# Kernel tuning notes

Hardware: AMD Instinct MI355X
Metric: run time of the kernel (lower is better)

## Reference

```python
import jax, jax.numpy as jnp
import numpy as np

BS, SEQ, ENC, DEC, HEADS, INTERM = 32, 2048, 512, 512, 8, 128
IH = INTERM * HEADS


def setup_inputs() -> dict:
    key = jax.random.key(0)
    ks = jax.random.split(key, 16)
    s = 0.02
    return {
        "enc": jax.random.normal(ks[0], (BS, SEQ, ENC), jnp.float32),
        "dec": jax.random.normal(ks[1], (BS, 1, DEC + ENC), jnp.float32),
        "kappa": jax.random.uniform(ks[2], (BS, 1, HEADS), jnp.float32),
        "mask": jnp.ones((BS, SEQ, 1), jnp.float32),
        "Wv": jax.random.normal(ks[3], (ENC, IH), jnp.float32) * s,
        "bv": jnp.zeros((IH,), jnp.float32),
        "Wq": jax.random.normal(ks[4], (DEC + ENC, IH), jnp.float32) * s,
        "bq": jnp.zeros((IH,), jnp.float32),
        "Wf": jax.random.normal(ks[5], (IH, HEADS), jnp.float32) * s,
        "bf": jnp.zeros((HEADS,), jnp.float32),
        "Wb": jax.random.normal(ks[6], (DEC + ENC, HEADS), jnp.float32) * s,
        "bb": jnp.zeros((HEADS,), jnp.float32),
        "Wk": jax.random.normal(ks[7], (DEC + ENC, HEADS), jnp.float32) * s,
        "bk": jnp.zeros((HEADS,), jnp.float32),
        "Wfc": jax.random.normal(ks[8], (ENC * HEADS, ENC), jnp.float32) * s,
        "bfc": jnp.zeros((ENC,), jnp.float32),
    }


def reference(enc, dec, kappa, mask, Wv, bv, Wq, bq, Wf, bf, Wb, bb, Wk, bk, Wfc, bfc):
    bs, seq_len, _ = enc.shape
    sp = jax.nn.softplus
    value = enc @ Wv + bv                      # (bs, seq, IH)
    query = dec @ Wq + bq                      # (bs, 1, IH), broadcasts over seq
    alpha = sp(jnp.tanh(query + value) @ Wf + bf) * mask   # (bs, seq, heads)
    beta = sp(dec @ Wb + bb)                   # (bs, 1, heads)
    kappa = kappa + sp(dec @ Wk + bk)          # (bs, 1, heads)
    u = jnp.arange(seq_len, dtype=enc.dtype)[None, :, None]
    score = alpha * jnp.exp(-beta * (kappa - u) ** 2)       # (bs, seq, heads)
    # weighted reduction over seq: (bs, heads, enc) then flatten in heads-major order
    context = jnp.einsum("bsh,bse->bhe", score, enc).reshape(bs, -1)
    context = context @ Wfc + bfc              # (bs, enc)
    return context[:, None, :], kappa, score
```

## Files before the change

### kernel.cpp

```cpp
#include <hip/hip_runtime.h>
#include <cstdint>
#include <cstddef>

#define BSZ    32
#define SEQL   2048
#define ENCD   512
#define DE     1024
#define NHEADS 8
#define IHD    1024

typedef unsigned short u16;
typedef __bf16 bf16x8 __attribute__((ext_vector_type(8)));
typedef float floatx4 __attribute__((ext_vector_type(4)));
typedef unsigned short u16x8 __attribute__((ext_vector_type(8)));

__device__ __forceinline__ u16 f2bf(float f) {
    unsigned int u = __float_as_uint(f);
    u = (u + 0x7FFFu + ((u >> 16) & 1u)) >> 16;
    return (u16)u;
}
__device__ __forceinline__ float bf2f(u16 v) {
    return __uint_as_float(((unsigned int)v) << 16);
}
__device__ __forceinline__ float softplus_f(float x) {
    return fmaxf(x, 0.0f) + log1pf(__expf(-fabsf(x)));
}
__device__ __forceinline__ float tanh_fast(float x) {
    const float e = __expf(2.0f * x);
    return 1.0f - 2.0f / (e + 1.0f);
}
__device__ __forceinline__ void async_cp16(u16* lds, const u16* g) {
    __builtin_amdgcn_global_load_lds(
        (const __attribute__((address_space(1))) unsigned int*)g,
        (__attribute__((address_space(3))) unsigned int*)lds, 16, 0, 0);
}

__global__ __launch_bounds__(256) void pre_kernel(
    const float* __restrict__ Wv, const float* __restrict__ Wf,
    u16* __restrict__ WvT, u16* __restrict__ wfb,
    const float* __restrict__ dec, const float* __restrict__ kappa_in,
    const float* __restrict__ Wq, const float* __restrict__ bq,
    const float* __restrict__ bv,
    const float* __restrict__ Wb, const float* __restrict__ bb,
    const float* __restrict__ Wk, const float* __restrict__ bk,
    float* __restrict__ query_ws, float* __restrict__ beta_ws,
    float* __restrict__ kappa_out)
{
    __shared__ float sh[64 * 65];
    const int bid = blockIdx.x, tid = threadIdx.x;

    if (bid < 128) {
        const int nt = bid & 15, kt = bid >> 4;
        for (int i = tid; i < 4096; i += 256) {
            const int kk = i >> 6, nn = i & 63;
            sh[kk * 65 + nn] = Wv[(size_t)(kt * 64 + kk) * IHD + nt * 64 + nn];
        }
        __syncthreads();
        for (int i = tid; i < 4096; i += 256) {
            const int nn = i >> 6, kk = i & 63;
            WvT[(size_t)(nt * 64 + nn) * 512 + kt * 64 + kk] = f2bf(sh[kk * 65 + nn]);
        }
        return;
    }
    if (bid == 128) {
        for (int i = tid; i < 8192; i += 256) {
            const int j   = i & 7;
            const int fr8 = (i >> 3) & 7;
            const int qd  = (i >> 6) & 3;
            const int ks  = (i >> 8) & 3;
            const int nn  = i >> 10;
            const int row = nn * 128 + ks * 32 + qd * 8 + j;
            wfb[i] = f2bf(Wf[row * NHEADS + fr8]);
        }
        return;
    }
    const int p = bid - 129;
    const int b = p & 31, y = p >> 5;
    float* s_dec = sh;
    float* s_red = sh + DE;
    for (int i = tid; i < DE; i += 256) s_dec[i] = dec[b * DE + i];
    __syncthreads();

    if (y < 32) {
        const int cl = tid & 31, kg = tid >> 5;
        const int col = y * 32 + cl;
        float a = 0.f;
        const float* w = Wq + col;
        #pragma unroll 8
        for (int k = kg * 128; k < kg * 128 + 128; ++k)
            a = fmaf(s_dec[k], w[(size_t)k * IHD], a);
        s_red[tid] = a;
        __syncthreads();
        if (tid < 32) {
            float s = 0.f;
            #pragma unroll
            for (int i = 0; i < 8; ++i) s += s_red[i * 32 + tid];
            query_ws[(size_t)b * IHD + col] = s + bq[col] + bv[col];
        }
    } else {
        const int h = tid & 7, kg = tid >> 3;
        float ab = 0.f, ak = 0.f;
        for (int k = kg * 32; k < kg * 32 + 32; ++k) {
            const float d = s_dec[k];
            ab = fmaf(d, Wb[k * NHEADS + h], ab);
            ak = fmaf(d, Wk[k * NHEADS + h], ak);
        }
        s_red[tid] = ab;
        __syncthreads();
        for (int off = 128; off >= 8; off >>= 1) {
            if (tid < off) s_red[tid] += s_red[tid + off];
            __syncthreads();
        }
        const float abT = (tid < 8) ? s_red[tid] : 0.f;
        __syncthreads();
        s_red[tid] = ak;
        __syncthreads();
        for (int off = 128; off >= 8; off >>= 1) {
            if (tid < off) s_red[tid] += s_red[tid + off];
            __syncthreads();
        }
        if (tid < 8) {
            beta_ws[b * NHEADS + tid]   = softplus_f(bb[tid] + abT);
            kappa_out[b * NHEADS + tid] = kappa_in[b * NHEADS + tid]
                                        + softplus_f(bk[tid] + s_red[tid]);
        }
    }
}

#define BM 128

__global__ __launch_bounds__(256, 2) void gemm_score_ctx_kernel(
    const float* __restrict__ enc, u16* __restrict__ encb,
    const u16* __restrict__ wvT,
    const u16* __restrict__ wfb2, const float* __restrict__ bf_g,
    const float* __restrict__ mask, const float* __restrict__ query_ws,
    const float* __restrict__ beta_ws, const float* __restrict__ kappa_out,
    float* __restrict__ score_out, float* __restrict__ ctx_part)
{
    __shared__ __align__(16) unsigned char smem[69632];
    u16*   tT      = (u16*)(smem + 32768);
    float* s_score = (float*)(smem + 65536);

    const int tid  = threadIdx.x;
    const int m0   = blockIdx.x * BM;
    const int b    = blockIdx.x >> 4;
    const int sc   = blockIdx.x & 15;
    const int lane = tid & 63;
    const int w    = tid >> 6;
    const int wr   = w >> 1, wc = w & 1;
    const int fr   = lane & 15, quad = lane >> 4;

    {
        const float4* src = (const float4*)enc + (size_t)m0 * 128;
        u16x8* dst = (u16x8*)(encb + (size_t)m0 * 512);
        #pragma unroll 4
        for (int i = tid; i < 8192; i += 256) {
            const float4 a = src[i * 2], b2 = src[i * 2 + 1];
            u16x8 o;
            o[0] = f2bf(a.x);  o[1] = f2bf(a.y);  o[2] = f2bf(a.z);  o[3] = f2bf(a.w);
            o[4] = f2bf(b2.x); o[5] = f2bf(b2.y); o[6] = f2bf(b2.z); o[7] = f2bf(b2.w);
            dst[i] = o;
        }
        asm volatile("s_waitcnt vmcnt(0)" ::: "memory");
        __builtin_amdgcn_sched_barrier(0);
        __builtin_amdgcn_s_barrier();
    }

    int mA[4], csA[4];
    #pragma unroll
    for (int r = 0; r < 4; ++r) {
        const int c = r * 256 + tid;
        mA[r]  = c >> 3;
        csA[r] = (c & 7) ^ (mA[r] & 7);
    }

    auto stage = [&](int bufsel, int it) {
        u16* Ab = (u16*)(smem + bufsel * 32768);
        u16* Bb = Ab + 8192;
        const int nn2 = it >> 3, kt2 = it & 7;
        const size_t aoff = (size_t)kt2 * 64;
        const size_t boff = (size_t)nn2 * (128 * 512) + (size_t)kt2 * 64;
        #pragma unroll
        for (int r = 0; r < 4; ++r) {
            async_cp16(Ab + (r * 256 + (tid & 192)) * 8,
                       encb + (size_t)(m0 + mA[r]) * 512 + aoff + csA[r] * 8);
            async_cp16(Bb + (size_t)(r * 256 + (tid & 192)) * 8,
                       wvT + (size_t)mA[r] * 512 + boff + csA[r] * 8);
        }
    };

    floatx4 acc2[2] = {};

    stage(0, 0);

    for (int nn = 0; nn < 8; ++nn) {
        const int n0 = nn * 128;
        float qv[4];
        bf16x8 wfr[4];
        floatx4 acc[4][4] = {};

        #pragma unroll
        for (int kt = 0; kt < 8; ++kt) {
            const int it = nn * 8 + kt;
            if (kt < 7 || nn < 7)
                stage((it + 1) & 1, it + 1);
            if (kt == 0) {
                #pragma unroll
                for (int nt = 0; nt < 4; ++nt)
                    qv[nt] = query_ws[(size_t)b * IHD + n0 + wc * 64 + nt * 16 + fr];
                #pragma unroll
                for (int ks = 0; ks < 4; ++ks)
                    wfr[ks] = *(const bf16x8*)&wfb2[((nn * 4 + ks) * 4 + quad) * 64
                                                    + (fr & 7) * 8];
            }
            if (kt == 7 && nn == 7) {
                asm volatile("s_waitcnt vmcnt(0)" ::: "memory");
            } else if (kt == 0) {
                asm volatile("s_waitcnt vmcnt(16)" ::: "memory");
            } else {
                asm volatile("s_waitcnt vmcnt(8)" ::: "memory");
            }
            __builtin_amdgcn_sched_barrier(0);
            __builtin_amdgcn_s_barrier();

            u16* Ab = (u16*)(smem + (it & 1) * 32768);
            u16* Bb = Ab + 8192;
            __builtin_amdgcn_s_setprio(1);
            #pragma unroll
            for (int s2 = 0; s2 < 2; ++s2) {
                bf16x8 af[4], bfr[4];
                #pragma unroll
                for (int mt = 0; mt < 4; ++mt) {
                    const int ma = wr * 64 + mt * 16 + fr;
                    const int ca = (s2 * 4 + quad) ^ (ma & 7);
                    af[mt] = *(const bf16x8*)&Ab[ma * 64 + ca * 8];
                }
                #pragma unroll
                for (int nt = 0; nt < 4; ++nt) {
                    const int nb = wc * 64 + nt * 16 + fr;
                    const int cb = (s2 * 4 + quad) ^ (nb & 7);
                    bfr[nt] = *(const bf16x8*)&Bb[nb * 64 + cb * 8];
                }
                #pragma unroll
                for (int mt = 0; mt < 4; ++mt)
                    #pragma unroll
                    for (int nt = 0; nt < 4; ++nt)
                        acc[mt][nt] = __builtin_amdgcn_mfma_f32_16x16x32_bf16(
                            af[mt], bfr[nt], acc[mt][nt], 0, 0, 0);
            }
            __builtin_amdgcn_s_setprio(0);
            __builtin_amdgcn_sched_barrier(0);
            __builtin_amdgcn_s_barrier();
        }

        #pragma unroll
        for (int mt = 0; mt < 4; ++mt) {
            #pragma unroll
            for (int nt = 0; nt < 4; ++nt) {
                const int col = wc * 64 + nt * 16 + fr;
                #pragma unroll
                for (int reg = 0; reg < 4; ++reg) {
                    const int row = wr * 64 + mt * 16 + quad * 4 + reg;
                    ((__bf16*)tT)[row * 128 + (col ^ ((row & 7) << 3))] =
                        (__bf16)tanh_fast(acc[mt][nt][reg] + qv[nt]);
                }
            }
        }
        asm volatile("s_waitcnt lgkmcnt(0)" ::: "memory");
        __builtin_amdgcn_sched_barrier(0);
        __builtin_amdgcn_s_barrier();

        #pragma unroll
        for (int t = 0; t < 2; ++t) {
            const int row = w * 32 + t * 16 + fr;
            #pragma unroll
            for (int ks = 0; ks < 4; ++ks) {
                const bf16x8 ta = *(const bf16x8*)
                    &tT[row * 128 + ((ks * 32 + quad * 8) ^ ((row & 7) << 3))];
                acc2[t] = __builtin_amdgcn_mfma_f32_16x16x32_bf16(ta, wfr[ks], acc2[t], 0, 0, 0);
            }
        }
        __builtin_amdgcn_sched_barrier(0);
        __builtin_amdgcn_s_barrier();
    }

    if (fr < NHEADS) {
        const float bfh = bf_g[fr];
        const float bet = beta_ws[b * NHEADS + fr];
        const float kap = kappa_out[b * NHEADS + fr];
        #pragma unroll
        for (int t = 0; t < 2; ++t) {
            #pragma unroll
            for (int reg = 0; reg < 4; ++reg) {
                const int row  = w * 32 + t * 16 + quad * 4 + reg;
                const int grow = m0 + row;
                const int s = grow & 2047;
                const float alpha = softplus_f(acc2[t][reg] + bfh) * mask[grow];
                const float du = kap - (float)s;
                s_score[row * NHEADS + fr] = alpha * __expf(-bet * du * du);
            }
        }
    }
    asm volatile("s_waitcnt lgkmcnt(0)" ::: "memory");
    __builtin_amdgcn_s_barrier();

    {
        const float4* src4 = (const float4*)s_score;
        float4* dst4 = (float4*)(score_out + (size_t)m0 * NHEADS);
        dst4[tid] = src4[tid];
    }

    {
        float acc0[8] = {}, acc1[8] = {};
        const u16* ep = encb + (size_t)m0 * 512 + lane * 8;
        for (int s0 = 0; s0 < 128; s0 += 16) {
            u16x8 ev[16];
            #pragma unroll
            for (int u = 0; u < 16; ++u)
                ev[u] = *(const u16x8*)(ep + (size_t)(s0 + u) * 512);
            #pragma unroll
            for (int u = 0; u < 16; ++u) {
                const float2 sc2 = *(const float2*)&s_score[(s0 + u) * NHEADS + 2 * w];
                #pragma unroll
                for (int j = 0; j < 8; ++j) {
                    const float e = bf2f(ev[u][j]);
                    acc0[j] = fmaf(sc2.x, e, acc0[j]);
                    acc1[j] = fmaf(sc2.y, e, acc1[j]);
                }
            }
        }
        const int e8 = lane * 8;
        float* outp = ctx_part + ((size_t)sc * BSZ + b) * (NHEADS * ENCD);
        *(float4*)&outp[(2 * w + 0) * ENCD + e8]     = make_float4(acc0[0], acc0[1], acc0[2], acc0[3]);
        *(float4*)&outp[(2 * w + 0) * ENCD + e8 + 4] = make_float4(acc0[4], acc0[5], acc0[6], acc0[7]);
        *(float4*)&outp[(2 * w + 1) * ENCD + e8]     = make_float4(acc1[0], acc1[1], acc1[2], acc1[3]);
        *(float4*)&outp[(2 * w + 1) * ENCD + e8 + 4] = make_float4(acc1[4], acc1[5], acc1[6], acc1[7]);
    }
}

__global__ __launch_bounds__(256) void ctx_reduce_kernel(
    const float* __restrict__ part, float* __restrict__ ctx_ws)
{
    const int i = blockIdx.x * 256 + threadIdx.x;
    float a = 0.f;
    #pragma unroll
    for (int sc = 0; sc < 16; ++sc)
        a += part[(size_t)sc * 131072 + i];
    ctx_ws[i] = a;
}

__global__ __launch_bounds__(256) void final_kernel(
    const float* __restrict__ ctx_ws, const float* __restrict__ Wfc,
    const float* __restrict__ bfc, float* __restrict__ out_ctx)
{
    __shared__ float s_ctx[32][128];
    const int jc = blockIdx.x, ks = blockIdx.y, tid = threadIdx.x;
    const int jl = tid & 31, bg = tid >> 5;
    const int j = jc * 32 + jl;
    const int k0 = ks * 128;

    for (int i = tid; i < 32 * 128; i += 256) {
        const int bb2 = i >> 7, kk = i & 127;
        s_ctx[bb2][kk] = ctx_ws[(size_t)bb2 * (NHEADS * ENCD) + k0 + kk];
    }
    __syncthreads();

    float a0 = 0.f, a1 = 0.f, a2 = 0.f, a3 = 0.f;
    for (int kk = 0; kk < 128; ++kk) {
        const float wv = Wfc[(size_t)(k0 + kk) * ENCD + j];
        a0 = fmaf(s_ctx[bg * 4 + 0][kk], wv, a0);
        a1 = fmaf(s_ctx[bg * 4 + 1][kk], wv, a1);
        a2 = fmaf(s_ctx[bg * 4 + 2][kk], wv, a2);
        a3 = fmaf(s_ctx[bg * 4 + 3][kk], wv, a3);
    }
    const float bias = (ks == 0) ? bfc[j] : 0.0f;
    atomicAdd(&out_ctx[(bg * 4 + 0) * ENCD + j], a0 + bias);
    atomicAdd(&out_ctx[(bg * 4 + 1) * ENCD + j], a1 + bias);
    atomicAdd(&out_ctx[(bg * 4 + 2) * ENCD + j], a2 + bias);
    atomicAdd(&out_ctx[(bg * 4 + 3) * ENCD + j], a3 + bias);
}

extern "C" void kernel_launch(void* const* d_in, const int* in_sizes, int n_in,
                              void* d_out, int out_size, void* d_ws, size_t ws_size,
                              hipStream_t stream)
{
    const float* enc   = (const float*)d_in[0];
    const float* dec   = (const float*)d_in[1];
    const float* kapin = (const float*)d_in[2];
    const float* mask  = (const float*)d_in[3];
    const float* Wv    = (const float*)d_in[4];
    const float* bv    = (const float*)d_in[5];
    const float* Wq    = (const float*)d_in[6];
    const float* bq    = (const float*)d_in[7];
    const float* Wf    = (const float*)d_in[8];
    const float* bf    = (const float*)d_in[9];
    const float* Wb    = (const float*)d_in[10];
    const float* bb    = (const float*)d_in[11];
    const float* Wk    = (const float*)d_in[12];
    const float* bk    = (const float*)d_in[13];
    const float* Wfc   = (const float*)d_in[14];
    const float* bfc   = (const float*)d_in[15];

    float* out       = (float*)d_out;
    float* out_ctx   = out;
    float* out_kappa = out + 16384;
    float* out_score = out + 16640;

    char* w = (char*)d_ws;
    u16*   enc_bf   = (u16*)w;
    float* ctx_part = (float*)(w + 67108864);
    u16*   wvT      = (u16*)(w + 75497472);
    float* q_ws     = (float*)(w + 76546048);
    float* beta_ws  = (float*)(w + 76677120);
    float* ctx_ws   = (float*)(w + 76678144);
    u16*   wfb      = (u16*)(w + 77202432);

    hipMemsetAsync(out_ctx, 0, 16384 * sizeof(float), stream);

    pre_kernel<<<dim3(128 + 1 + 1056), dim3(256), 0, stream>>>(
        Wv, Wf, wvT, wfb,
        dec, kapin, Wq, bq, bv, Wb, bb, Wk, bk, q_ws, beta_ws, out_kappa);

    gemm_score_ctx_kernel<<<dim3((BSZ * SEQL) / BM), dim3(256), 0, stream>>>(
        enc, enc_bf, wvT, wfb, bf, mask, q_ws, beta_ws, out_kappa,
        out_score, ctx_part);

    ctx_reduce_kernel<<<dim3(512), dim3(256), 0, stream>>>(ctx_part, ctx_ws);

    final_kernel<<<dim3(16, 32), dim3(256), 0, stream>>>(
        ctx_ws, Wfc, bfc, out_ctx);
}
```

Measured before the change: 393.2 us.

## Fuse fp32-to-bf16 encoder conversion into first GEMM pass pipeline

The separate prologue that converts the block's encoder rows to bf16 and writes them to global memory is removed. During the first n-tile pass, each A tile is loaded as fp32 into registers, converted, and written both to LDS and to the bf16 global scratch, with the wait counts adjusted. Later passes keep the original async bf16 copy path. This aims to overlap the conversion with MFMA work and drop a full-block barrier, at the cost of more register pressure and fragile vmcnt bookkeeping.

```diff
diff --git a/kernel.cpp b/kernel.cpp
--- a/kernel.cpp
+++ b/kernel.cpp
@@ -150,22 +150,6 @@
     const int wr   = w >> 1, wc = w & 1;
     const int fr   = lane & 15, quad = lane >> 4;
 
-    {
-        const float4* src = (const float4*)enc + (size_t)m0 * 128;
-        u16x8* dst = (u16x8*)(encb + (size_t)m0 * 512);
-        #pragma unroll 4
-        for (int i = tid; i < 8192; i += 256) {
-            const float4 a = src[i * 2], b2 = src[i * 2 + 1];
-            u16x8 o;
-            o[0] = f2bf(a.x);  o[1] = f2bf(a.y);  o[2] = f2bf(a.z);  o[3] = f2bf(a.w);
-            o[4] = f2bf(b2.x); o[5] = f2bf(b2.y); o[6] = f2bf(b2.z); o[7] = f2bf(b2.w);
-            dst[i] = o;
-        }
-        asm volatile("s_waitcnt vmcnt(0)" ::: "memory");
-        __builtin_amdgcn_sched_barrier(0);
-        __builtin_amdgcn_s_barrier();
-    }
-
     int mA[4], csA[4];
     #pragma unroll
     for (int r = 0; r < 4; ++r) {
@@ -174,7 +158,38 @@
         csA[r] = (c & 7) ^ (mA[r] & 7);
     }
 
-    auto stage = [&](int bufsel, int it) {
+    float4 a0[4], a1[4];
+
+    auto loadAf32 = [&](int kt2) {
+        #pragma unroll
+        for (int r = 0; r < 4; ++r) {
+            const float* s = enc + (size_t)(m0 + mA[r]) * 512 + kt2 * 64 + csA[r] * 8;
+            a0[r] = *(const float4*)s;
+            a1[r] = *(const float4*)(s + 4);
+        }
+    };
+    auto writeStoreA = [&](int sel, int kt2) {
+        u16* Ab = (u16*)(smem + sel * 32768);
+        #pragma unroll
+        for (int r = 0; r < 4; ++r) {
+            u16x8 o;
+            o[0] = f2bf(a0[r].x); o[1] = f2bf(a0[r].y);
+            o[2] = f2bf(a0[r].z); o[3] = f2bf(a0[r].w);
+            o[4] = f2bf(a1[r].x); o[5] = f2bf(a1[r].y);
+            o[6] = f2bf(a1[r].z); o[7] = f2bf(a1[r].w);
+            *(u16x8*)&Ab[(size_t)(r * 256 + tid) * 8] = o;
+            *(u16x8*)&encb[(size_t)(m0 + mA[r]) * 512 + kt2 * 64 + csA[r] * 8] = o;
+        }
+    };
+    auto stageBonly = [&](int sel, int kt2) {
+        u16* Bb = (u16*)(smem + sel * 32768) + 8192;
+        const u16* src = wvT + (size_t)kt2 * 64;
+        #pragma unroll
+        for (int r = 0; r < 4; ++r)
+            async_cp16(Bb + (r * 256 + (tid & 192)) * 8,
+                       src + (size_t)mA[r] * 512 + csA[r] * 8);
+    };
+    auto stageAB = [&](int bufsel, int it) {
         u16* Ab = (u16*)(smem + bufsel * 32768);
         u16* Bb = Ab + 8192;
         const int nn2 = it >> 3, kt2 = it & 7;
@@ -191,7 +206,13 @@
 
     floatx4 acc2[2] = {};
 
-    stage(0, 0);
+    loadAf32(0);
+    stageBonly(0, 0);
+    asm volatile("s_waitcnt vmcnt(4)" ::: "memory");
+    __builtin_amdgcn_sched_barrier(0);
+    writeStoreA(0, 0);
+    asm volatile("s_waitcnt lgkmcnt(0)" ::: "memory");
+    __builtin_amdgcn_sched_barrier(0);
 
     for (int nn = 0; nn < 8; ++nn) {
         const int n0 = nn * 128;
@@ -202,8 +223,13 @@
         #pragma unroll
         for (int kt = 0; kt < 8; ++kt) {
             const int it = nn * 8 + kt;
-            if (kt < 7 || nn < 7)
-                stage((it + 1) & 1, it + 1);
+            if (nn == 0) {
+                if (kt < 7) { loadAf32(kt + 1); stageBonly((kt + 1) & 1, kt + 1); }
+                else        { stageAB(0, 8); }
+            } else {
+                if (kt < 7 || nn < 7)
+                    stageAB((it + 1) & 1, it + 1);
+            }
             if (kt == 0) {
                 #pragma unroll
                 for (int nt = 0; nt < 4; ++nt)
@@ -213,12 +239,14 @@
                     wfr[ks] = *(const bf16x8*)&wfb2[((nn * 4 + ks) * 4 + quad) * 64
                                                     + (fr & 7) * 8];
             }
-            if (kt == 7 && nn == 7) {
-                asm volatile("s_waitcnt vmcnt(0)" ::: "memory");
-            } else if (kt == 0) {
-                asm volatile("s_waitcnt vmcnt(16)" ::: "memory");
+            if (nn == 0) {
+                if (kt == 0)      { asm volatile("s_waitcnt vmcnt(20)" ::: "memory"); }
+                else if (kt == 7) { asm volatile("s_waitcnt vmcnt(8)"  ::: "memory"); }
+                else              { asm volatile("s_waitcnt vmcnt(12)" ::: "memory"); }
             } else {
-                asm volatile("s_waitcnt vmcnt(8)" ::: "memory");
+                if (kt == 7 && nn == 7) { asm volatile("s_waitcnt vmcnt(0)"  ::: "memory"); }
+                else if (kt == 0)       { asm volatile("s_waitcnt vmcnt(16)" ::: "memory"); }
+                else                    { asm volatile("s_waitcnt vmcnt(8)"  ::: "memory"); }
             }
             __builtin_amdgcn_sched_barrier(0);
             __builtin_amdgcn_s_barrier();
@@ -250,6 +278,15 @@
             }
             __builtin_amdgcn_s_setprio(0);
             __builtin_amdgcn_sched_barrier(0);
+
+            if (nn == 0 && kt < 7) {
+                if (kt == 0) { asm volatile("s_waitcnt vmcnt(12)" ::: "memory"); }
+                else         { asm volatile("s_waitcnt vmcnt(4)"  ::: "memory"); }
+                __builtin_amdgcn_sched_barrier(0);
+                writeStoreA((kt + 1) & 1, kt + 1);
+                asm volatile("s_waitcnt lgkmcnt(0)" ::: "memory");
+                __builtin_amdgcn_sched_barrier(0);
+            }
             __builtin_amdgcn_s_barrier();
         }
 
```

New measurement: 451.3 us. 14.8% more time.
